# Kernel optimization log

Measured on AMD Instinct MI355X. Metric: run time of the kernel, lower is better.

The kernel has to match this reference:

```python
import jax, jax.numpy as jnp
import numpy as np

BETA = 0.25  # commitment_weight


def _conv(x, w, b=None, stride=1, pad=0):
    y = jax.lax.conv_general_dilated(x, w, (stride, stride), ((pad, pad), (pad, pad)),
                                     dimension_numbers=('NCHW', 'OIHW', 'NCHW'))
    return y if b is None else y + b[None, :, None, None]


def _convT(x, w, b):
    # PyTorch ConvTranspose2d(kernel=4, stride=2, padding=1); w stored as (in, out, 4, 4)
    wf = jnp.flip(w, (2, 3)).transpose(1, 0, 2, 3)  # -> OIHW, spatially flipped
    y = jax.lax.conv_general_dilated(x, wf, (1, 1), ((2, 2), (2, 2)), lhs_dilation=(2, 2),
                                     dimension_numbers=('NCHW', 'OIHW', 'NCHW'))
    return y + b[None, :, None, None]


def _res(x, wa, wb):
    # ResidualLayer: x + conv1x1(relu(conv3x3(x))) , both convs bias-free
    return x + _conv(jax.nn.relu(_conv(x, wa, pad=1)), wb)


def _lrelu(x):
    return jax.nn.leaky_relu(x, 0.01)


def setup_inputs() -> dict:
    key = jax.random.key(0)
    ks = iter(jax.random.split(key, 32))
    def p(shape, s=0.05):
        return jax.random.normal(next(ks), shape, jnp.float32) * s
    inp = {
        'inputs': jax.random.normal(next(ks), (16, 4, 256, 256), jnp.float32),
        # encoder
        'e1_w': p((64, 4, 4, 4)),    'e1_b': p((64,)),
        'e2_w': p((128, 64, 4, 4)),  'e2_b': p((128,)),
        'e3_w': p((128, 128, 3, 3)), 'e3_b': p((128,)),
        'r1a_w': p((128, 128, 3, 3)), 'r1b_w': p((128, 128, 1, 1)),
        'r2a_w': p((128, 128, 3, 3)), 'r2b_w': p((128, 128, 1, 1)),
        'e4_w': p((64, 128, 1, 1)),  'e4_b': p((64,)),
        # residual VQ codebooks: (num_quantizers, codebook_size, dim)
        'codebooks': p((4, 512, 64), 1.0),
        # decoder
        'd1_w': p((128, 64, 3, 3)),  'd1_b': p((128,)),
        'dr1a_w': p((128, 128, 3, 3)), 'dr1b_w': p((128, 128, 1, 1)),
        'dr2a_w': p((128, 128, 3, 3)), 'dr2b_w': p((128, 128, 1, 1)),
        'dt1_w': p((128, 64, 4, 4)), 'dt1_b': p((64,)),  # (in, out, kH, kW) torch layout
        'dt2_w': p((64, 4, 4, 4)),   'dt2_b': p((4,)),
    }
    return inp


def reference(inputs, e1_w, e1_b, e2_w, e2_b, e3_w, e3_b, r1a_w, r1b_w, r2a_w, r2b_w,
              e4_w, e4_b, codebooks, d1_w, d1_b, dr1a_w, dr1b_w, dr2a_w, dr2b_w,
              dt1_w, dt1_b, dt2_w, dt2_b):
    # ---- encoder ----
    h = _lrelu(_conv(inputs, e1_w, e1_b, 2, 1))
    h = _lrelu(_conv(h, e2_w, e2_b, 2, 1))
    h = _lrelu(_conv(h, e3_w, e3_b, 1, 1))
    h = _res(h, r1a_w, r1b_w)
    h = _res(h, r2a_w, r2b_w)
    h = _lrelu(h)
    h = _lrelu(_conv(h, e4_w, e4_b, 1, 0))
    # ---- residual vector quantization ----
    z = h.transpose(0, 2, 3, 1)                     # B,H,W,D
    B, H, W, D = z.shape
    r = z.reshape(-1, D)                            # N,D tokens
    q_out = jnp.zeros_like(r)
    idx_list, losses = [], []
    for i in range(codebooks.shape[0]):
        cb = codebooks[i]                           # K,D
        d = (r * r).sum(-1, keepdims=True) - 2.0 * (r @ cb.T) + (cb * cb).sum(-1)
        idx = jnp.argmin(d, axis=-1)                # N
        q = cb[idx]                                 # N,D gather
        losses.append(BETA * jnp.mean((jax.lax.stop_gradient(q) - r) ** 2))
        q_st = r + jax.lax.stop_gradient(q - r)     # straight-through
        q_out = q_out + q_st
        r = r - jax.lax.stop_gradient(q)            # residual for next stage
        idx_list.append(idx)
    indices = jnp.stack(idx_list, -1).reshape(B, H, W, -1)   # B,H,W,Q
    losses = jnp.stack(losses)                                # (Q,)
    qz = q_out.reshape(B, H, W, D).transpose(0, 3, 1, 2)      # B,D,H,W
    # ---- decoder ----
    h = _lrelu(_conv(qz, d1_w, d1_b, 1, 1))
    h = _res(h, dr1a_w, dr1b_w)
    h = _res(h, dr2a_w, dr2b_w)
    h = _lrelu(h)
    h = _lrelu(_convT(h, dt1_w, dt1_b))
    recons = jax.nn.relu(_convT(h, dt2_w, dt2_b))
    return recons, indices, losses
```

## Files before the change

kernel.cpp:

```cpp
#include <hip/hip_runtime.h>
#include <cstddef>


template<int ACT> __device__ __forceinline__ float actf(float v) {
    if constexpr (ACT == 1) return v > 0.f ? v : 0.f;
    else if constexpr (ACT == 2) return v > 0.f ? v : 0.01f * v;
    else return v;
}
__device__ __forceinline__ float lrelu_in(float v) { return v > 0.f ? v : 0.01f * v; }

template<int CIN, int COUT, int K, int S, int P, int HIN, int WIN, int HOUT, int WOUT,
         int ICC, int NPY, int ACT, bool BIAS>
__launch_bounds__(256, (NPY >= 4 ? 2 : 4))
__global__ void conv_k(const float* __restrict__ in, const float* __restrict__ w,
                       const float* __restrict__ bias, float* __restrict__ out)
{
    constexpr int K2 = K * K;
    constexpr int NR = S * (NPY - 1) + K;
    constexpr int BH = 16 * NPY;
    __shared__ float sw[ICC * K2 * 16];
    const int tid = threadIdx.x;
    const int tx = tid & 15, ty = tid >> 4;
    constexpr int TW = WOUT / 16;
    const int bx = blockIdx.x % TW, by = blockIdx.x / TW;
    const int ox = bx * 16 + tx;
    const int oy0 = by * BH + ty * NPY;
    const int oc0 = blockIdx.y * 16;
    const int n = blockIdx.z;
    const int ix0 = ox * S - P, iy0 = oy0 * S - P;

    int ro[NR]; float mr[NR];
#pragma unroll
    for (int r = 0; r < NR; ++r) {
        const int iy = iy0 + r;
        const bool v = (iy >= 0) && (iy < HIN);
        ro[r] = v ? iy * WIN : 0;
        mr[r] = v ? 1.f : 0.f;
    }
    int co[K]; float mc[K];
#pragma unroll
    for (int c = 0; c < K; ++c) {
        const int ix = ix0 + c;
        const bool v = (ix >= 0) && (ix < WIN);
        co[c] = v ? ix : 0;
        mc[c] = v ? 1.f : 0.f;
    }

    float acc[NPY][16];
#pragma unroll
    for (int py = 0; py < NPY; ++py)
#pragma unroll
        for (int j = 0; j < 16; ++j) acc[py][j] = 0.f;

    for (int ic0 = 0; ic0 < CIN; ic0 += ICC) {
        __syncthreads();
        for (int t = tid; t < ICC * K2 * 16; t += 256) {
            int oc_l = t & 15, r = t >> 4, k = r % K2, ic_l = r / K2;
            sw[(ic_l * K2 + k) * 16 + oc_l] =
                w[((size_t)(oc0 + oc_l) * CIN + ic0 + ic_l) * K2 + k];
        }
        __syncthreads();
#pragma unroll 1
        for (int ic_l = 0; ic_l < ICC; ++ic_l) {
            const float* ip = in + (size_t)(n * CIN + ic0 + ic_l) * HIN * WIN;
            float patch[NR][K];
#pragma unroll
            for (int r = 0; r < NR; ++r)
#pragma unroll
                for (int c = 0; c < K; ++c)
                    patch[r][c] = ip[ro[r] + co[c]] * (mr[r] * mc[c]);
            const float* swp = &sw[ic_l * K2 * 16];
#pragma unroll
            for (int ky = 0; ky < K; ++ky) {
#pragma unroll
                for (int kx = 0; kx < K; ++kx) {
                    const float4* wp = (const float4*)&swp[(ky * K + kx) * 16];
                    float4 w0 = wp[0], w1 = wp[1], w2 = wp[2], w3 = wp[3];
#pragma unroll
                    for (int py = 0; py < NPY; ++py) {
                        const float v = patch[py * S + ky][kx];
                        acc[py][0]  = fmaf(w0.x, v, acc[py][0]);
                        acc[py][1]  = fmaf(w0.y, v, acc[py][1]);
                        acc[py][2]  = fmaf(w0.z, v, acc[py][2]);
                        acc[py][3]  = fmaf(w0.w, v, acc[py][3]);
                        acc[py][4]  = fmaf(w1.x, v, acc[py][4]);
                        acc[py][5]  = fmaf(w1.y, v, acc[py][5]);
                        acc[py][6]  = fmaf(w1.z, v, acc[py][6]);
                        acc[py][7]  = fmaf(w1.w, v, acc[py][7]);
                        acc[py][8]  = fmaf(w2.x, v, acc[py][8]);
                        acc[py][9]  = fmaf(w2.y, v, acc[py][9]);
                        acc[py][10] = fmaf(w2.z, v, acc[py][10]);
                        acc[py][11] = fmaf(w2.w, v, acc[py][11]);
                        acc[py][12] = fmaf(w3.x, v, acc[py][12]);
                        acc[py][13] = fmaf(w3.y, v, acc[py][13]);
                        acc[py][14] = fmaf(w3.z, v, acc[py][14]);
                        acc[py][15] = fmaf(w3.w, v, acc[py][15]);
                    }
                }
            }
        }
    }
#pragma unroll
    for (int py = 0; py < NPY; ++py) {
#pragma unroll
        for (int j = 0; j < 16; ++j) {
            float r = acc[py][j];
            if (BIAS) r += bias[oc0 + j];
            r = actf<ACT>(r);
            out[((size_t)(n * COUT + oc0 + j) * HOUT + oy0 + py) * WOUT + ox] = r;
        }
    }
}

template<int CIN, int COUT, int NPX, int ACT, bool BIAS, bool INL, bool RESID, bool TOK>
__launch_bounds__(256, 3)
__global__ void conv1x1_k(const float* __restrict__ in, const float* __restrict__ w,
                          const float* __restrict__ bias, const float* __restrict__ resid,
                          float* __restrict__ out)
{
    constexpr int HW = 4096;
    __shared__ float sw[16 * CIN];
    const int tid = threadIdx.x;
    const int base = blockIdx.x * (256 * NPX) + tid;
    const int oc0 = blockIdx.y * 16;
    const int n = blockIdx.z;

    for (int t = tid; t < 16 * CIN; t += 256) {
        int oc_l = t & 15, ic = t >> 4;
        sw[ic * 16 + oc_l] = w[(size_t)(oc0 + oc_l) * CIN + ic];
    }
    __syncthreads();

    float acc[NPX][16];
#pragma unroll
    for (int p = 0; p < NPX; ++p)
#pragma unroll
        for (int j = 0; j < 16; ++j) acc[p][j] = 0.f;

    const float* ip = in + (size_t)n * CIN * HW;
#pragma unroll 2
    for (int ic = 0; ic < CIN; ++ic) {
        float v[NPX];
#pragma unroll
        for (int p = 0; p < NPX; ++p) {
            float t = ip[(size_t)ic * HW + base + 256 * p];
            if (INL) t = lrelu_in(t);
            v[p] = t;
        }
        const float4* wp = (const float4*)&sw[ic * 16];
#pragma unroll
        for (int q4 = 0; q4 < 4; ++q4) {
            const float4 wv = wp[q4];
#pragma unroll
            for (int p = 0; p < NPX; ++p) {
                acc[p][q4 * 4 + 0] = fmaf(wv.x, v[p], acc[p][q4 * 4 + 0]);
                acc[p][q4 * 4 + 1] = fmaf(wv.y, v[p], acc[p][q4 * 4 + 1]);
                acc[p][q4 * 4 + 2] = fmaf(wv.z, v[p], acc[p][q4 * 4 + 2]);
                acc[p][q4 * 4 + 3] = fmaf(wv.w, v[p], acc[p][q4 * 4 + 3]);
            }
        }
    }
#pragma unroll
    for (int p = 0; p < NPX; ++p) {
        const int pix = base + 256 * p;
#pragma unroll
        for (int j = 0; j < 16; ++j) {
            float r = acc[p][j];
            if (BIAS) r += bias[oc0 + j];
            r = actf<ACT>(r);
            if (RESID) r += resid[((size_t)(n * COUT + oc0 + j)) * HW + pix];
            if (TOK)
                out[((size_t)n * HW + pix) * COUT + oc0 + j] = r;
            else
                out[((size_t)(n * COUT + oc0 + j)) * HW + pix] = r;
        }
    }
}

template<int CIN, int COUT, int OCT, int HIN, int ICC, int ACT, bool INL>
__launch_bounds__(256, 3)
__global__ void convt_k(const float* __restrict__ in, const float* __restrict__ w,
                        const float* __restrict__ bias, float* __restrict__ out)
{
    constexpr int WIN = HIN, HOUT = 2 * HIN, WOUT = 2 * HIN;
    __shared__ float sw[ICC * 16 * OCT];
    const int tid = threadIdx.x;
    const int tx = tid & 15, ty = tid >> 4;
    constexpr int TBW = WOUT / 32;
    const int bx = blockIdx.x % TBW, by = blockIdx.x / TBW;
    const int A = by * 16 + ty;
    const int C = bx * 16 + tx;
    const int oc0 = blockIdx.y * OCT;
    const int n = blockIdx.z;

    int offs[9]; float msk[9];
#pragma unroll
    for (int dy = 0; dy < 3; ++dy) {
#pragma unroll
        for (int dx = 0; dx < 3; ++dx) {
            const int iy = A - 1 + dy, ix = C - 1 + dx;
            const bool v = (iy >= 0) && (iy < HIN) && (ix >= 0) && (ix < WIN);
            offs[dy * 3 + dx] = v ? iy * WIN + ix : 0;
            msk[dy * 3 + dx] = v ? 1.f : 0.f;
        }
    }

    float acc[4 * OCT];
#pragma unroll
    for (int j = 0; j < 4 * OCT; ++j) acc[j] = 0.f;

    for (int ic0 = 0; ic0 < CIN; ic0 += ICC) {
        __syncthreads();
        for (int t = tid; t < ICC * 16 * OCT; t += 256) {
            int oc_l = t % OCT, r = t / OCT, k = r & 15, ic_l = r >> 4;
            sw[(ic_l * 16 + k) * OCT + oc_l] =
                w[((size_t)(ic0 + ic_l) * COUT + oc0 + oc_l) * 16 + k];
        }
        __syncthreads();
#pragma unroll 1
        for (int ic_l = 0; ic_l < ICC; ++ic_l) {
            const float* ip = in + (size_t)(n * CIN + ic0 + ic_l) * HIN * WIN;
            float in9[9];
#pragma unroll
            for (int j = 0; j < 9; ++j) {
                float v = ip[offs[j]] * msk[j];
                if (INL) v = lrelu_in(v);
                in9[j] = v;
            }
#pragma unroll
            for (int ky = 0; ky < 4; ++ky) {
                const int ry = (ky + 1) & 1;
                const int dy = 2 - ((ky + 1) >> 1);
#pragma unroll
                for (int kx = 0; kx < 4; ++kx) {
                    const int rx = (kx + 1) & 1;
                    const int dx = 2 - ((kx + 1) >> 1);
                    const float v = in9[dy * 3 + dx];
                    const int po = ry * 2 + rx;
                    const float4* wp = (const float4*)&sw[(ic_l * 16 + ky * 4 + kx) * OCT];
#pragma unroll
                    for (int q4 = 0; q4 < OCT / 4; ++q4) {
                        float4 wv = wp[q4];
                        acc[po * OCT + q4 * 4 + 0] = fmaf(wv.x, v, acc[po * OCT + q4 * 4 + 0]);
                        acc[po * OCT + q4 * 4 + 1] = fmaf(wv.y, v, acc[po * OCT + q4 * 4 + 1]);
                        acc[po * OCT + q4 * 4 + 2] = fmaf(wv.z, v, acc[po * OCT + q4 * 4 + 2]);
                        acc[po * OCT + q4 * 4 + 3] = fmaf(wv.w, v, acc[po * OCT + q4 * 4 + 3]);
                    }
                }
            }
        }
    }
#pragma unroll
    for (int po = 0; po < 4; ++po) {
        const int ry = po >> 1, rx = po & 1;
        const int oy = 2 * A + ry, ox = 2 * C + rx;
#pragma unroll
        for (int j = 0; j < OCT; ++j) {
            float r = acc[po * OCT + j] + bias[oc0 + j];
            r = actf<ACT>(r);
            out[((size_t)(n * COUT + oc0 + j) * HOUT + oy) * WOUT + ox] = r;
        }
    }
}

__global__ void norm_k(const float* __restrict__ cb, float* __restrict__ nrm) {
    const int c = blockIdx.x * 256 + threadIdx.x;
    const float4* p = (const float4*)(cb + (size_t)c * 64);
    float a0 = 0.f, a1 = 0.f, a2 = 0.f, a3 = 0.f;
#pragma unroll
    for (int i = 0; i < 16; ++i) {
        float4 v = p[i];
        a0 = fmaf(v.x, v.x, a0); a1 = fmaf(v.y, v.y, a1);
        a2 = fmaf(v.z, v.z, a2); a3 = fmaf(v.w, v.w, a3);
    }
    nrm[c] = (a0 + a1) + (a2 + a3);
}

__launch_bounds__(128, 2)
__global__ void rvq_k(const float* __restrict__ z, const float* __restrict__ cb,
                      const float* __restrict__ nrm,
                      float* __restrict__ q, float* __restrict__ idx_out,
                      float* __restrict__ loss_acc)
{
    __shared__ float lds_min[2][64];
    __shared__ int   lds_idx[2][64];
    const int tid = threadIdx.x;
    const int lane = tid & 63;
    const int w = __builtin_amdgcn_readfirstlane(tid >> 6);
    const int t = blockIdx.x * 64 + lane;

    float r[64];
    {
        const float4* zp = (const float4*)(z + (size_t)t * 64);
#pragma unroll
        for (int i = 0; i < 16; ++i) {
            float4 v = zp[i];
            r[4 * i + 0] = v.x; r[4 * i + 1] = v.y;
            r[4 * i + 2] = v.z; r[4 * i + 3] = v.w;
        }
    }

    for (int s = 0; s < 4; ++s) {
        float sr2;
        {
            float a0 = 0.f, a1 = 0.f, a2 = 0.f, a3 = 0.f;
            float b0 = 0.f, b1 = 0.f, b2 = 0.f, b3 = 0.f;
#pragma unroll
            for (int i = 0; i < 32; i += 4) {
                a0 = fmaf(r[i + 0], r[i + 0], a0);
                a1 = fmaf(r[i + 1], r[i + 1], a1);
                a2 = fmaf(r[i + 2], r[i + 2], a2);
                a3 = fmaf(r[i + 3], r[i + 3], a3);
                b0 = fmaf(r[32 + i + 0], r[32 + i + 0], b0);
                b1 = fmaf(r[32 + i + 1], r[32 + i + 1], b1);
                b2 = fmaf(r[32 + i + 2], r[32 + i + 2], b2);
                b3 = fmaf(r[32 + i + 3], r[32 + i + 3], b3);
            }
            sr2 = ((a0 + a1) + (a2 + a3)) + ((b0 + b1) + (b2 + b3));
        }

        const float* cbase = cb + ((size_t)s * 512 + (size_t)w * 256) * 64;
        const float* nbase = nrm + s * 512 + w * 256;
        float dmin = 3.4e38f;
        int best = 0;
#pragma unroll 2
        for (int kk = 0; kk < 256; ++kk) {
            const float4* cp = (const float4*)(cbase + (size_t)kk * 64);
            float a0 = 0.f, a1 = 0.f, a2 = 0.f, a3 = 0.f;
            float b0 = 0.f, b1 = 0.f, b2 = 0.f, b3 = 0.f;
#pragma unroll
            for (int i = 0; i < 8; ++i) {
                float4 c = cp[i];
                a0 = fmaf(r[4 * i + 0], c.x, a0);
                a1 = fmaf(r[4 * i + 1], c.y, a1);
                a2 = fmaf(r[4 * i + 2], c.z, a2);
                a3 = fmaf(r[4 * i + 3], c.w, a3);
            }
#pragma unroll
            for (int i = 0; i < 8; ++i) {
                float4 c = cp[8 + i];
                b0 = fmaf(r[32 + 4 * i + 0], c.x, b0);
                b1 = fmaf(r[32 + 4 * i + 1], c.y, b1);
                b2 = fmaf(r[32 + 4 * i + 2], c.z, b2);
                b3 = fmaf(r[32 + 4 * i + 3], c.w, b3);
            }
            const float dot = ((a0 + a1) + (a2 + a3)) + ((b0 + b1) + (b2 + b3));
            const float d = fmaf(-2.f, dot, sr2) + nbase[kk];
            if (d < dmin) { dmin = d; best = kk; }
        }
        best += w * 256;

        lds_min[w][lane] = dmin;
        lds_idx[w][lane] = best;
        __syncthreads();
        const float dA = lds_min[0][lane]; const int iA = lds_idx[0][lane];
        const float dB = lds_min[1][lane]; const int iB = lds_idx[1][lane];
        __syncthreads();
        const bool takeB = dB < dA;
        dmin = takeB ? dB : dA;
        best = takeB ? iB : iA;

        if (w == 0) {
            idx_out[(size_t)t * 4 + s] = (float)best;
            float lv = dmin;
#pragma unroll
            for (int off = 32; off; off >>= 1) lv += __shfl_down(lv, off, 64);
            if (lane == 0) atomicAdd(&loss_acc[s], lv);
        }

        const float4* cbest = (const float4*)(cb + ((size_t)s * 512 + best) * 64);
#pragma unroll
        for (int i = 0; i < 16; ++i) {
            float4 c = cbest[i];
            r[4 * i + 0] -= c.x; r[4 * i + 1] -= c.y;
            r[4 * i + 2] -= c.z; r[4 * i + 3] -= c.w;
        }
    }

    if (w == 0) {
        const float4* zp = (const float4*)(z + (size_t)t * 64);
        const int n = t >> 12, pix = t & 4095;
        float* qp = q + (size_t)n * 64 * 4096 + pix;
#pragma unroll
        for (int i = 0; i < 16; ++i) {
            float4 v = zp[i];
            qp[(size_t)(4 * i + 0) * 4096] = v.x - r[4 * i + 0];
            qp[(size_t)(4 * i + 1) * 4096] = v.y - r[4 * i + 1];
            qp[(size_t)(4 * i + 2) * 4096] = v.z - r[4 * i + 2];
            qp[(size_t)(4 * i + 3) * 4096] = v.w - r[4 * i + 3];
        }
    }
}

__global__ void init_k(float* loss_acc) {
    if (threadIdx.x < 4) loss_acc[threadIdx.x] = 0.f;
}
__global__ void fin_k(const float* __restrict__ loss_acc, float* __restrict__ out_loss) {
    if (threadIdx.x < 4)
        out_loss[threadIdx.x] = loss_acc[threadIdx.x] * (0.25f / 4194304.f);
}

extern "C" void kernel_launch(void* const* d_in, const int* in_sizes, int n_in,
                              void* d_out, int out_size, void* d_ws, size_t ws_size,
                              hipStream_t stream)
{
    const float* x    = (const float*)d_in[0];
    const float* e1w  = (const float*)d_in[1];  const float* e1b = (const float*)d_in[2];
    const float* e2w  = (const float*)d_in[3];  const float* e2b = (const float*)d_in[4];
    const float* e3w  = (const float*)d_in[5];  const float* e3b = (const float*)d_in[6];
    const float* r1aw = (const float*)d_in[7];  const float* r1bw = (const float*)d_in[8];
    const float* r2aw = (const float*)d_in[9];  const float* r2bw = (const float*)d_in[10];
    const float* e4w  = (const float*)d_in[11]; const float* e4b = (const float*)d_in[12];
    const float* cbs  = (const float*)d_in[13];
    const float* d1w  = (const float*)d_in[14]; const float* d1b = (const float*)d_in[15];
    const float* dr1aw= (const float*)d_in[16]; const float* dr1bw = (const float*)d_in[17];
    const float* dr2aw= (const float*)d_in[18]; const float* dr2bw = (const float*)d_in[19];
    const float* dt1w = (const float*)d_in[20]; const float* dt1b = (const float*)d_in[21];
    const float* dt2w = (const float*)d_in[22]; const float* dt2b = (const float*)d_in[23];

    float* out = (float*)d_out;
    float* ws  = (float*)d_ws;

    float* BIG = ws;
    float* P2  = BIG;
    float* P3  = BIG + 8388608;
    float* P1  = ws + 16777216;
    float* Z   = ws + 25165824;
    float* Q   = ws + 29360128;
    float* LACC= ws + 33554432;
    float* NRM = ws + 33554448;

    float* out_recons = out;
    float* out_idx    = out + 4194304;
    float* out_loss   = out + 4194304 + 262144;

    init_k<<<1, 64, 0, stream>>>(LACC);
    norm_k<<<8, 256, 0, stream>>>(cbs, NRM);

    conv_k<4, 64, 4, 2, 1, 256, 256, 128, 128, 4, 2, 2, true>
        <<<dim3(32, 4, 16), 256, 0, stream>>>(x, e1w, e1b, BIG);
    conv_k<64, 128, 4, 2, 1, 128, 128, 64, 64, 16, 2, 2, true>
        <<<dim3(8, 8, 16), 256, 0, stream>>>(BIG, e2w, e2b, P1);
    conv_k<128, 128, 3, 1, 1, 64, 64, 64, 64, 16, 4, 2, true>
        <<<dim3(4, 8, 16), 256, 0, stream>>>(P1, e3w, e3b, P2);
    conv_k<128, 128, 3, 1, 1, 64, 64, 64, 64, 16, 4, 1, false>
        <<<dim3(4, 8, 16), 256, 0, stream>>>(P2, r1aw, nullptr, P3);
    conv1x1_k<128, 128, 4, 0, false, false, true, false>
        <<<dim3(4, 8, 16), 256, 0, stream>>>(P3, r1bw, nullptr, P2, P1);
    conv_k<128, 128, 3, 1, 1, 64, 64, 64, 64, 16, 4, 1, false>
        <<<dim3(4, 8, 16), 256, 0, stream>>>(P1, r2aw, nullptr, P3);
    conv1x1_k<128, 128, 4, 0, false, false, true, false>
        <<<dim3(4, 8, 16), 256, 0, stream>>>(P3, r2bw, nullptr, P1, P2);
    conv1x1_k<128, 64, 2, 2, true, true, false, true>
        <<<dim3(8, 4, 16), 256, 0, stream>>>(P2, e4w, e4b, nullptr, Z);

    rvq_k<<<1024, 128, 0, stream>>>(Z, cbs, NRM, Q, out_idx, LACC);
    fin_k<<<1, 64, 0, stream>>>(LACC, out_loss);

    conv_k<64, 128, 3, 1, 1, 64, 64, 64, 64, 16, 4, 2, true>
        <<<dim3(4, 8, 16), 256, 0, stream>>>(Q, d1w, d1b, P1);
    conv_k<128, 128, 3, 1, 1, 64, 64, 64, 64, 16, 4, 1, false>
        <<<dim3(4, 8, 16), 256, 0, stream>>>(P1, dr1aw, nullptr, P2);
    conv1x1_k<128, 128, 4, 0, false, false, true, false>
        <<<dim3(4, 8, 16), 256, 0, stream>>>(P2, dr1bw, nullptr, P1, P3);
    conv_k<128, 128, 3, 1, 1, 64, 64, 64, 64, 16, 4, 1, false>
        <<<dim3(4, 8, 16), 256, 0, stream>>>(P3, dr2aw, nullptr, P2);
    conv1x1_k<128, 128, 4, 0, false, false, true, false>
        <<<dim3(4, 8, 16), 256, 0, stream>>>(P2, dr2bw, nullptr, P3, P1);
    convt_k<128, 64, 16, 64, 8, 2, true>
        <<<dim3(16, 4, 16), 256, 0, stream>>>(P1, dt1w, dt1b, BIG);
    convt_k<64, 4, 4, 128, 16, 1, false>
        <<<dim3(64, 1, 16), 256, 0, stream>>>(BIG, dt2w, dt2b, out_recons);
}
```

Measured before the change: 2.995 ms.

## Stage RVQ codebook chunks in LDS and process two tokens per thread

The residual VQ kernel now copies 128-row codebook chunks (64 rows per wave half) plus their norms into shared memory over four passes, and each thread handles two tokens at once. Every codebook value read from LDS is reused for two dot products, and global codebook traffic is shared across the block instead of being re-read by each wave. The grid is halved to match. The cost is 128 live residual registers per thread, which raises register pressure and may cause spills or lower occupancy, plus extra barriers for each chunk load.

```diff
diff --git a/kernel.cpp b/kernel.cpp
--- a/kernel.cpp
+++ b/kernel.cpp
@@ -282,112 +282,183 @@
                       float* __restrict__ q, float* __restrict__ idx_out,
                       float* __restrict__ loss_acc)
 {
-    __shared__ float lds_min[2][64];
-    __shared__ int   lds_idx[2][64];
+    __shared__ float scb[128 * 64];
+    __shared__ float snrm[128];
+    __shared__ float lmin[2][2][64];
+    __shared__ int   lidx[2][2][64];
     const int tid = threadIdx.x;
     const int lane = tid & 63;
     const int w = __builtin_amdgcn_readfirstlane(tid >> 6);
-    const int t = blockIdx.x * 64 + lane;
-
-    float r[64];
+    const int w64 = w * 64;
+    const int t0 = blockIdx.x * 128 + lane;
+    const int t1 = t0 + 64;
+
+    float r0[64], r1[64];
     {
-        const float4* zp = (const float4*)(z + (size_t)t * 64);
+        const float4* zp0 = (const float4*)(z + (size_t)t0 * 64);
+        const float4* zp1 = (const float4*)(z + (size_t)t1 * 64);
 #pragma unroll
         for (int i = 0; i < 16; ++i) {
-            float4 v = zp[i];
-            r[4 * i + 0] = v.x; r[4 * i + 1] = v.y;
-            r[4 * i + 2] = v.z; r[4 * i + 3] = v.w;
+            float4 v = zp0[i];
+            r0[4 * i + 0] = v.x; r0[4 * i + 1] = v.y;
+            r0[4 * i + 2] = v.z; r0[4 * i + 3] = v.w;
+            float4 u = zp1[i];
+            r1[4 * i + 0] = u.x; r1[4 * i + 1] = u.y;
+            r1[4 * i + 2] = u.z; r1[4 * i + 3] = u.w;
         }
     }
 
     for (int s = 0; s < 4; ++s) {
-        float sr2;
+        float sr20, sr21;
         {
             float a0 = 0.f, a1 = 0.f, a2 = 0.f, a3 = 0.f;
             float b0 = 0.f, b1 = 0.f, b2 = 0.f, b3 = 0.f;
 #pragma unroll
             for (int i = 0; i < 32; i += 4) {
-                a0 = fmaf(r[i + 0], r[i + 0], a0);
-                a1 = fmaf(r[i + 1], r[i + 1], a1);
-                a2 = fmaf(r[i + 2], r[i + 2], a2);
-                a3 = fmaf(r[i + 3], r[i + 3], a3);
-                b0 = fmaf(r[32 + i + 0], r[32 + i + 0], b0);
-                b1 = fmaf(r[32 + i + 1], r[32 + i + 1], b1);
-                b2 = fmaf(r[32 + i + 2], r[32 + i + 2], b2);
-                b3 = fmaf(r[32 + i + 3], r[32 + i + 3], b3);
-            }
-            sr2 = ((a0 + a1) + (a2 + a3)) + ((b0 + b1) + (b2 + b3));
-        }
-
-        const float* cbase = cb + ((size_t)s * 512 + (size_t)w * 256) * 64;
-        const float* nbase = nrm + s * 512 + w * 256;
-        float dmin = 3.4e38f;
-        int best = 0;
-#pragma unroll 2
-        for (int kk = 0; kk < 256; ++kk) {
-            const float4* cp = (const float4*)(cbase + (size_t)kk * 64);
+                a0 = fmaf(r0[i + 0], r0[i + 0], a0);
+                a1 = fmaf(r0[i + 1], r0[i + 1], a1);
+                a2 = fmaf(r0[i + 2], r0[i + 2], a2);
+                a3 = fmaf(r0[i + 3], r0[i + 3], a3);
+                b0 = fmaf(r0[32 + i + 0], r0[32 + i + 0], b0);
+                b1 = fmaf(r0[32 + i + 1], r0[32 + i + 1], b1);
+                b2 = fmaf(r0[32 + i + 2], r0[32 + i + 2], b2);
+                b3 = fmaf(r0[32 + i + 3], r0[32 + i + 3], b3);
+            }
+            sr20 = ((a0 + a1) + (a2 + a3)) + ((b0 + b1) + (b2 + b3));
+        }
+        {
             float a0 = 0.f, a1 = 0.f, a2 = 0.f, a3 = 0.f;
             float b0 = 0.f, b1 = 0.f, b2 = 0.f, b3 = 0.f;
 #pragma unroll
-            for (int i = 0; i < 8; ++i) {
-                float4 c = cp[i];
-                a0 = fmaf(r[4 * i + 0], c.x, a0);
-                a1 = fmaf(r[4 * i + 1], c.y, a1);
-                a2 = fmaf(r[4 * i + 2], c.z, a2);
-                a3 = fmaf(r[4 * i + 3], c.w, a3);
-            }
-#pragma unroll
-            for (int i = 0; i < 8; ++i) {
-                float4 c = cp[8 + i];
-                b0 = fmaf(r[32 + 4 * i + 0], c.x, b0);
-                b1 = fmaf(r[32 + 4 * i + 1], c.y, b1);
-                b2 = fmaf(r[32 + 4 * i + 2], c.z, b2);
-                b3 = fmaf(r[32 + 4 * i + 3], c.w, b3);
-            }
-            const float dot = ((a0 + a1) + (a2 + a3)) + ((b0 + b1) + (b2 + b3));
-            const float d = fmaf(-2.f, dot, sr2) + nbase[kk];
-            if (d < dmin) { dmin = d; best = kk; }
-        }
-        best += w * 256;
-
-        lds_min[w][lane] = dmin;
-        lds_idx[w][lane] = best;
+            for (int i = 0; i < 32; i += 4) {
+                a0 = fmaf(r1[i + 0], r1[i + 0], a0);
+                a1 = fmaf(r1[i + 1], r1[i + 1], a1);
+                a2 = fmaf(r1[i + 2], r1[i + 2], a2);
+                a3 = fmaf(r1[i + 3], r1[i + 3], a3);
+                b0 = fmaf(r1[32 + i + 0], r1[32 + i + 0], b0);
+                b1 = fmaf(r1[32 + i + 1], r1[32 + i + 1], b1);
+                b2 = fmaf(r1[32 + i + 2], r1[32 + i + 2], b2);
+                b3 = fmaf(r1[32 + i + 3], r1[32 + i + 3], b3);
+            }
+            sr21 = ((a0 + a1) + (a2 + a3)) + ((b0 + b1) + (b2 + b3));
+        }
+
+        float dmin0 = 3.4e38f, dmin1 = 3.4e38f;
+        int best0 = 0, best1 = 0;
+
+        for (int pass = 0; pass < 4; ++pass) {
+            __syncthreads();
+            {
+                const float4* csrc = (const float4*)(cb + (size_t)s * 512 * 64);
+                for (int i = tid; i < 2048; i += 128) {
+                    const int row = i >> 4, f4 = i & 15;
+                    const int grow = pass * 64 + row + ((row & 64) * 3);
+                    ((float4*)scb)[row * 16 + f4] = csrc[(size_t)grow * 16 + f4];
+                }
+                const int g = pass * 64 + tid + ((tid & 64) * 3);
+                snrm[tid] = nrm[s * 512 + g];
+            }
+            __syncthreads();
+
+#pragma unroll 2
+            for (int kk = 0; kk < 64; ++kk) {
+                const float4* cp = (const float4*)&scb[(size_t)(w64 + kk) * 64];
+                float a0 = 0.f, a1 = 0.f, a2 = 0.f, a3 = 0.f;
+                float e0 = 0.f, e1 = 0.f, e2 = 0.f, e3 = 0.f;
+#pragma unroll
+                for (int i = 0; i < 8; ++i) {
+                    float4 c = cp[i];
+                    a0 = fmaf(r0[4 * i + 0], c.x, a0);
+                    a1 = fmaf(r0[4 * i + 1], c.y, a1);
+                    a2 = fmaf(r0[4 * i + 2], c.z, a2);
+                    a3 = fmaf(r0[4 * i + 3], c.w, a3);
+                    e0 = fmaf(r1[4 * i + 0], c.x, e0);
+                    e1 = fmaf(r1[4 * i + 1], c.y, e1);
+                    e2 = fmaf(r1[4 * i + 2], c.z, e2);
+                    e3 = fmaf(r1[4 * i + 3], c.w, e3);
+                }
+                float b0 = 0.f, b1 = 0.f, b2 = 0.f, b3 = 0.f;
+                float f0 = 0.f, f1 = 0.f, f2 = 0.f, f3 = 0.f;
+#pragma unroll
+                for (int i = 0; i < 8; ++i) {
+                    float4 c = cp[8 + i];
+                    b0 = fmaf(r0[32 + 4 * i + 0], c.x, b0);
+                    b1 = fmaf(r0[32 + 4 * i + 1], c.y, b1);
+                    b2 = fmaf(r0[32 + 4 * i + 2], c.z, b2);
+                    b3 = fmaf(r0[32 + 4 * i + 3], c.w, b3);
+                    f0 = fmaf(r1[32 + 4 * i + 0], c.x, f0);
+                    f1 = fmaf(r1[32 + 4 * i + 1], c.y, f1);
+                    f2 = fmaf(r1[32 + 4 * i + 2], c.z, f2);
+                    f3 = fmaf(r1[32 + 4 * i + 3], c.w, f3);
+                }
+                const float dot0 = ((a0 + a1) + (a2 + a3)) + ((b0 + b1) + (b2 + b3));
+                const float dot1 = ((e0 + e1) + (e2 + e3)) + ((f0 + f1) + (f2 + f3));
+                const float nk = snrm[w64 + kk];
+                const float d0 = fmaf(-2.f, dot0, sr20) + nk;
+                const float d1 = fmaf(-2.f, dot1, sr21) + nk;
+                const int kl = pass * 64 + kk;
+                if (d0 < dmin0) { dmin0 = d0; best0 = kl; }
+                if (d1 < dmin1) { dmin1 = d1; best1 = kl; }
+            }
+        }
+
+        lmin[w][0][lane] = dmin0; lidx[w][0][lane] = best0 + w * 256;
+        lmin[w][1][lane] = dmin1; lidx[w][1][lane] = best1 + w * 256;
         __syncthreads();
-        const float dA = lds_min[0][lane]; const int iA = lds_idx[0][lane];
-        const float dB = lds_min[1][lane]; const int iB = lds_idx[1][lane];
-        __syncthreads();
-        const bool takeB = dB < dA;
-        dmin = takeB ? dB : dA;
-        best = takeB ? iB : iA;
-
-        if (w == 0) {
-            idx_out[(size_t)t * 4 + s] = (float)best;
-            float lv = dmin;
+        const float dA0 = lmin[0][0][lane], dB0 = lmin[1][0][lane];
+        const int   iA0 = lidx[0][0][lane], iB0 = lidx[1][0][lane];
+        const float dA1 = lmin[0][1][lane], dB1 = lmin[1][1][lane];
+        const int   iA1 = lidx[0][1][lane], iB1 = lidx[1][1][lane];
+        const bool tB0 = dB0 < dA0;
+        const bool tB1 = dB1 < dA1;
+        const float d0c = tB0 ? dB0 : dA0;  const int b0c = tB0 ? iB0 : iA0;
+        const float d1c = tB1 ? dB1 : dA1;  const int b1c = tB1 ? iB1 : iA1;
+
+        {
+            float lv = (w == 0) ? d0c : d1c;
 #pragma unroll
             for (int off = 32; off; off >>= 1) lv += __shfl_down(lv, off, 64);
             if (lane == 0) atomicAdd(&loss_acc[s], lv);
         }
-
-        const float4* cbest = (const float4*)(cb + ((size_t)s * 512 + best) * 64);
+        if (w == 0) idx_out[(size_t)t0 * 4 + s] = (float)b0c;
+        else        idx_out[(size_t)t1 * 4 + s] = (float)b1c;
+
+        const float4* c0 = (const float4*)(cb + ((size_t)s * 512 + b0c) * 64);
+        const float4* c1 = (const float4*)(cb + ((size_t)s * 512 + b1c) * 64);
 #pragma unroll
         for (int i = 0; i < 16; ++i) {
-            float4 c = cbest[i];
-            r[4 * i + 0] -= c.x; r[4 * i + 1] -= c.y;
-            r[4 * i + 2] -= c.z; r[4 * i + 3] -= c.w;
+            float4 v = c0[i];
+            r0[4 * i + 0] -= v.x; r0[4 * i + 1] -= v.y;
+            r0[4 * i + 2] -= v.z; r0[4 * i + 3] -= v.w;
+            float4 u = c1[i];
+            r1[4 * i + 0] -= u.x; r1[4 * i + 1] -= u.y;
+            r1[4 * i + 2] -= u.z; r1[4 * i + 3] -= u.w;
         }
     }
 
     if (w == 0) {
-        const float4* zp = (const float4*)(z + (size_t)t * 64);
-        const int n = t >> 12, pix = t & 4095;
+        const float4* zp = (const float4*)(z + (size_t)t0 * 64);
+        const int n = t0 >> 12, pix = t0 & 4095;
         float* qp = q + (size_t)n * 64 * 4096 + pix;
 #pragma unroll
         for (int i = 0; i < 16; ++i) {
             float4 v = zp[i];
-            qp[(size_t)(4 * i + 0) * 4096] = v.x - r[4 * i + 0];
-            qp[(size_t)(4 * i + 1) * 4096] = v.y - r[4 * i + 1];
-            qp[(size_t)(4 * i + 2) * 4096] = v.z - r[4 * i + 2];
-            qp[(size_t)(4 * i + 3) * 4096] = v.w - r[4 * i + 3];
+            qp[(size_t)(4 * i + 0) * 4096] = v.x - r0[4 * i + 0];
+            qp[(size_t)(4 * i + 1) * 4096] = v.y - r0[4 * i + 1];
+            qp[(size_t)(4 * i + 2) * 4096] = v.z - r0[4 * i + 2];
+            qp[(size_t)(4 * i + 3) * 4096] = v.w - r0[4 * i + 3];
+        }
+    } else {
+        const float4* zp = (const float4*)(z + (size_t)t1 * 64);
+        const int n = t1 >> 12, pix = t1 & 4095;
+        float* qp = q + (size_t)n * 64 * 4096 + pix;
+#pragma unroll
+        for (int i = 0; i < 16; ++i) {
+            float4 v = zp[i];
+            qp[(size_t)(4 * i + 0) * 4096] = v.x - r1[4 * i + 0];
+            qp[(size_t)(4 * i + 1) * 4096] = v.y - r1[4 * i + 1];
+            qp[(size_t)(4 * i + 2) * 4096] = v.z - r1[4 * i + 2];
+            qp[(size_t)(4 * i + 3) * 4096] = v.w - r1[4 * i + 3];
         }
     }
 }
@@ -454,7 +525,7 @@
     conv1x1_k<128, 64, 2, 2, true, true, false, true>
         <<<dim3(8, 4, 16), 256, 0, stream>>>(P2, e4w, e4b, nullptr, Z);
 
-    rvq_k<<<1024, 128, 0, stream>>>(Z, cbs, NRM, Q, out_idx, LACC);
+    rvq_k<<<512, 128, 0, stream>>>(Z, cbs, NRM, Q, out_idx, LACC);
     fin_k<<<1, 64, 0, stream>>>(LACC, out_loss);
 
     conv_k<64, 128, 3, 1, 1, 64, 64, 64, 64, 16, 4, 2, true>
```

Result: no change. 2.955 ms (-1.3%).
